# Kernel tuning notes

Measured on AMD Instinct MI355X. Metric: run time of the kernel, lower is better.

## Reference

```python
import jax, jax.numpy as jnp
import numpy as np

EPS = 1e-08
N_NODES = 100000
E_HALF = 3200000  # directed edges before symmetrization


def setup_inputs() -> dict:
    key = jax.random.key(0)
    k1, k2, k3 = jax.random.split(key, 3)
    pos = jax.random.normal(k1, (N_NODES, 3), dtype=jnp.float32)
    phi = jax.random.normal(k2, (N_NODES,), dtype=jnp.float32)
    e = jax.random.randint(k3, (2, E_HALF), 0, N_NODES, dtype=jnp.int32)
    # symmetrize (the torch module calls to_undirected); build undirected edge list
    edge_index = jnp.concatenate([e, e[::-1]], axis=1)  # (2, 2*E_HALF)
    return {"pos": pos, "phi": phi, "edge_index": edge_index}


def reference(pos, phi, edge_index):
    # pos: (N, 3), phi: (N,), edge_index: (2, E) already undirected
    n = pos.shape[0]
    row, col = edge_index[0], edge_index[1]
    dx = pos[col] - pos[row]                      # (E, 3)
    dphi = phi[col] - phi[row]                    # (E,)
    w = 1.0 / (jnp.linalg.norm(dx, axis=1) + EPS) ** 2  # (E,)
    outer = dx[:, :, None] * dx[:, None, :]      # (E, 3, 3)
    A = jax.ops.segment_sum(w[:, None, None] * outer, row, num_segments=n)  # (N,3,3)
    b = jax.ops.segment_sum((w * dphi)[:, None] * dx, row, num_segments=n)  # (N,3)
    A_reg = A + EPS * jnp.eye(3, dtype=pos.dtype)[None, :, :]
    grad_phi = jnp.linalg.solve(A_reg, b[..., None])[..., 0]  # (N,3)
    return grad_phi
```

## Files before the change

kernel.cpp:

```cpp
#include <hip/hip_runtime.h>
#include <hip/hip_bf16.h>
#include <math.h>

#define LSQ_EPS 1e-8f
#define BUCKET_BITS 7
#define BUCKET_SIZE 128
#define NB_MAX 800
#define CAP 8960
#define SCAT_BLOCKS 1024
#define STAGE_CAP 6272
#define VEC_ITERS 4
#define KV 5

__device__ __forceinline__ int hget(const unsigned int* hp, int b) {
    return (int)((hp[b >> 1] >> ((b & 1) * 16)) & 0xFFFFu);
}
__device__ __forceinline__ unsigned int hinc_rank(unsigned int* hp, int b) {
    unsigned int o = atomicAdd(&hp[b >> 1], 1u << ((b & 1) * 16));
    return (o >> ((b & 1) * 16)) & 0xFFFFu;
}

__global__ __launch_bounds__(256, 5) void lsq_scatter_sorted(
    const float* __restrict__ pos, const float* __restrict__ phi,
    const int* __restrict__ eidx, int E, int N, int NB,
    float4* __restrict__ pp4,
    unsigned int* __restrict__ region, int* __restrict__ g_cursor)
{
    __shared__ unsigned int staged[STAGE_CAP];
    __shared__ unsigned int histp[NB_MAX / 2];
    __shared__ unsigned short base16[NB_MAX];
    __shared__ unsigned short sstart16[NB_MAX];

    const int tid = threadIdx.x;
    const int E2 = E >> 1;

    for (int i = blockIdx.x * 256 + tid; i < N; i += SCAT_BLOCKS * 256)
        pp4[i] = make_float4(pos[3 * i + 0], pos[3 * i + 1], pos[3 * i + 2], phi[i]);

    int chunk = (E2 + SCAT_BLOCKS - 1) / SCAT_BLOCKS;
    chunk = (chunk + 3) & ~3;
    const int start = blockIdx.x * chunk;
    const int end = min(start + chunk, E2);
    if (start >= E2) return;

    for (int t = tid; t < NB_MAX / 2; t += 256) histp[t] = 0;
    __syncthreads();

    const int nvec = (end - start) & ~3;
    unsigned int rkA[VEC_ITERS][4];
    int4 rA[VEC_ITERS], cA[VEC_ITERS];
#pragma unroll
    for (int k = 0; k < VEC_ITERS; ++k) {
        int e = start + (tid << 2) + (k << 10);
        if (e < start + nvec) {
            int4 r = *(const int4*)(eidx + e);
            int4 c = *(const int4*)(eidx + E + e);
            rA[k] = r;
            cA[k] = c;
            rkA[k][0] = hinc_rank(histp, r.x >> BUCKET_BITS) |
                        (hinc_rank(histp, c.x >> BUCKET_BITS) << 16);
            rkA[k][1] = hinc_rank(histp, r.y >> BUCKET_BITS) |
                        (hinc_rank(histp, c.y >> BUCKET_BITS) << 16);
            rkA[k][2] = hinc_rank(histp, r.z >> BUCKET_BITS) |
                        (hinc_rank(histp, c.z >> BUCKET_BITS) << 16);
            rkA[k][3] = hinc_rank(histp, r.w >> BUCKET_BITS) |
                        (hinc_rank(histp, c.w >> BUCKET_BITS) << 16);
        }
    }
    unsigned int rkT = 0;
    int trow = 0, tcol = 0;
    const int tcnt = (end - start) - nvec;
    if (tid < tcnt) {
        int e = start + nvec + tid;
        trow = eidx[e];
        tcol = eidx[E + e];
        rkT = hinc_rank(histp, trow >> BUCKET_BITS) |
              (hinc_rank(histp, tcol >> BUCKET_BITS) << 16);
    }
    __syncthreads();

    int bs0 = 0, bs1 = 0, bs2 = 0, bs3 = 0;
    {
        int b = tid;
        if (b < NB) { int c = hget(histp, b); if (c > 0) bs0 = atomicAdd(&g_cursor[b], c); }
        b += 256;
        if (b < NB) { int c = hget(histp, b); if (c > 0) bs1 = atomicAdd(&g_cursor[b], c); }
        b += 256;
        if (b < NB) { int c = hget(histp, b); if (c > 0) bs2 = atomicAdd(&g_cursor[b], c); }
        b += 256;
        if (b < NB) { int c = hget(histp, b); if (c > 0) bs3 = atomicAdd(&g_cursor[b], c); }
    }
    if (tid < 64) {
        int carry = 0;
        for (int bi = 0; bi < NB; bi += 64) {
            int b = bi + tid;
            int c = (b < NB) ? hget(histp, b) : 0;
            int x = c;
#pragma unroll
            for (int d = 1; d < 64; d <<= 1) {
                int y = __shfl_up(x, d, 64);
                if (tid >= d) x += y;
            }
            if (b < NB) sstart16[b] = (unsigned short)(carry + x - c);
            carry += __shfl(x, 63, 64);
        }
    }
    asm volatile("s_waitcnt lgkmcnt(0)" ::: "memory");
    __builtin_amdgcn_s_barrier();

#pragma unroll
    for (int k = 0; k < VEC_ITERS; ++k) {
        int e = start + (tid << 2) + (k << 10);
        if (e < start + nvec) {
            int rr[4] = {rA[k].x, rA[k].y, rA[k].z, rA[k].w};
            int cc[4] = {cA[k].x, cA[k].y, cA[k].z, cA[k].w};
#pragma unroll
            for (int q = 0; q < 4; ++q) {
                int b1 = rr[q] >> BUCKET_BITS;
                int s1 = (int)sstart16[b1] + (int)(rkA[k][q] & 0xFFFFu);
                staged[s1] = ((unsigned int)(rr[q] & (BUCKET_SIZE - 1)) << 17) | (unsigned int)cc[q];
                int b2 = cc[q] >> BUCKET_BITS;
                int s2 = (int)sstart16[b2] + (int)(rkA[k][q] >> 16);
                staged[s2] = ((unsigned int)(cc[q] & (BUCKET_SIZE - 1)) << 17) | (unsigned int)rr[q];
            }
        }
    }
    if (tid < tcnt) {
        int b1 = trow >> BUCKET_BITS;
        staged[(int)sstart16[b1] + (int)(rkT & 0xFFFFu)] =
            ((unsigned int)(trow & (BUCKET_SIZE - 1)) << 17) | (unsigned int)tcol;
        int b2 = tcol >> BUCKET_BITS;
        staged[(int)sstart16[b2] + (int)(rkT >> 16)] =
            ((unsigned int)(tcol & (BUCKET_SIZE - 1)) << 17) | (unsigned int)trow;
    }

    if (tid < NB)       base16[tid]       = (unsigned short)min(bs0, 65535);
    if (tid + 256 < NB) base16[tid + 256] = (unsigned short)min(bs1, 65535);
    if (tid + 512 < NB) base16[tid + 512] = (unsigned short)min(bs2, 65535);
    if (tid + 768 < NB) base16[tid + 768] = (unsigned short)min(bs3, 65535);
    __syncthreads();

    {
        const int wv = tid >> 6, ln = tid & 63;
        const int grp = ln >> 3;
        const int sub = ln & 7;
        for (int b = wv * 8 + grp; b < NB; b += 32) {
            int cnt_b = hget(histp, b);
            if (cnt_b == 0) continue;
            int src = (int)sstart16[b];
            int dst = (int)base16[b];
            int kmax = min(cnt_b, CAP - dst);
            if (kmax <= 0) continue;
            unsigned int* dstp = region + (size_t)b * CAP + dst;
            const unsigned int* srcp = staged + src;
            for (int j = sub; j < kmax; j += 8)
                dstp[j] = srcp[j];
        }
    }
}

#define LSQ_ACC(qv)                                                            \
    {                                                                          \
        float dx = (qv).x - me.x;                                              \
        float dy = (qv).y - me.y;                                              \
        float dz = (qv).z - me.z;                                              \
        float dphi = (qv).w - me.w;                                            \
        float nn = sqrtf(dx * dx + dy * dy + dz * dz) + LSQ_EPS;               \
        float w = 1.0f / (nn * nn);                                            \
        float wd = w * dphi;                                                   \
        a00 += w * dx * dx; a01 += w * dx * dy; a02 += w * dx * dz;            \
        a11 += w * dy * dy; a12 += w * dy * dz; a22 += w * dz * dz;            \
        bb0 += wd * dx;     bb1 += wd * dy;     bb2 += wd * dz;                \
    }

__global__ __launch_bounds__(512, 6) void lsq_bucket_reduce(
    const float4* __restrict__ pp4,
    const unsigned int* __restrict__ region, const int* __restrict__ g_cursor,
    float* __restrict__ out, int N)
{
    __shared__ unsigned int sorted32[CAP];
    __shared__ int cnt[BUCKET_SIZE];
    __shared__ int startx[BUCKET_SIZE];

    const int b = blockIdx.x;
    const int tid = threadIdx.x;
    const int node_base = b << BUCKET_BITS;

    if (tid < BUCKET_SIZE) cnt[tid] = 0;
    __syncthreads();

    int count = g_cursor[b];
    if (count > CAP) count = CAP;
    const unsigned int* reg = region + (size_t)b * CAP;

    uint4 pcv[KV];
#pragma unroll
    for (int k = 0; k < KV; ++k) {
        int i = (tid << 2) + (k << 11);
        if (i < count) {
            uint4 p = *(const uint4*)(reg + i);
            unsigned int o0 = (unsigned int)atomicAdd(&cnt[p.x >> 17], 1);
            pcv[k].x = p.x | (o0 << 24);
            if (i + 1 < count) {
                unsigned int o1 = (unsigned int)atomicAdd(&cnt[p.y >> 17], 1);
                pcv[k].y = p.y | (o1 << 24);
            }
            if (i + 2 < count) {
                unsigned int o2 = (unsigned int)atomicAdd(&cnt[p.z >> 17], 1);
                pcv[k].z = p.z | (o2 << 24);
            }
            if (i + 3 < count) {
                unsigned int o3 = (unsigned int)atomicAdd(&cnt[p.w >> 17], 1);
                pcv[k].w = p.w | (o3 << 24);
            }
        }
    }
    __syncthreads();

    if (tid < 64) {
        int c0 = cnt[tid];
        int c1 = cnt[tid + 64];
        int x0 = c0, x1 = c1;
#pragma unroll
        for (int d = 1; d < 64; d <<= 1) {
            int y0 = __shfl_up(x0, d, 64);
            int y1 = __shfl_up(x1, d, 64);
            if (tid >= d) { x0 += y0; x1 += y1; }
        }
        int tot0 = __shfl(x0, 63, 64);
        startx[tid] = x0 - c0;
        startx[tid + 64] = tot0 + x1 - c1;
    }
    __syncthreads();

#pragma unroll
    for (int k = 0; k < KV; ++k) {
        int i = (tid << 2) + (k << 11);
        if (i < count) {
            unsigned int p0 = pcv[k].x;
            sorted32[startx[(p0 >> 17) & 0x7Fu] + (int)(p0 >> 24)] = p0 & 0x1FFFFu;
            if (i + 1 < count) {
                unsigned int p1 = pcv[k].y;
                sorted32[startx[(p1 >> 17) & 0x7Fu] + (int)(p1 >> 24)] = p1 & 0x1FFFFu;
            }
            if (i + 2 < count) {
                unsigned int p2 = pcv[k].z;
                sorted32[startx[(p2 >> 17) & 0x7Fu] + (int)(p2 >> 24)] = p2 & 0x1FFFFu;
            }
            if (i + 3 < count) {
                unsigned int p3 = pcv[k].w;
                sorted32[startx[(p3 >> 17) & 0x7Fu] + (int)(p3 >> 24)] = p3 & 0x1FFFFu;
            }
        }
    }
    __syncthreads();

    const int n = tid >> 2;
    const int qid = tid & 3;
    int node = node_base + n;
    float4 me = pp4[node < N ? node : 0];
    const int s = startx[n];
    const int cN = cnt[n];
    int lo = s + (cN * qid) / 4;
    const int hi = s + (cN * (qid + 1)) / 4;

    float a00 = 0, a01 = 0, a02 = 0, a11 = 0, a12 = 0, a22 = 0;
    float bb0 = 0, bb1 = 0, bb2 = 0;

    int i = lo;
    float4 q0, q1, q2, q3;
    bool have = (i + 3 < hi);
    if (have) {
        int c0 = (int)sorted32[i];
        int c1 = (int)sorted32[i + 1];
        int c2 = (int)sorted32[i + 2];
        int c3 = (int)sorted32[i + 3];
        q0 = pp4[c0]; q1 = pp4[c1]; q2 = pp4[c2]; q3 = pp4[c3];
    }
    while (have) {
        const int j = i + 4;
        const bool nhave = (j + 3 < hi);
        float4 p0, p1, p2, p3;
        if (nhave) {
            int c0 = (int)sorted32[j];
            int c1 = (int)sorted32[j + 1];
            int c2 = (int)sorted32[j + 2];
            int c3 = (int)sorted32[j + 3];
            p0 = pp4[c0]; p1 = pp4[c1]; p2 = pp4[c2]; p3 = pp4[c3];
        }
        LSQ_ACC(q0); LSQ_ACC(q1); LSQ_ACC(q2); LSQ_ACC(q3);
        q0 = p0; q1 = p1; q2 = p2; q3 = p3;
        i = j;
        have = nhave;
    }
    for (; i < hi; ++i) {
        int c0 = (int)sorted32[i];
        float4 qt = pp4[c0];
        LSQ_ACC(qt);
    }

    a00 += __shfl_down(a00, 1); a01 += __shfl_down(a01, 1);
    a02 += __shfl_down(a02, 1); a11 += __shfl_down(a11, 1);
    a12 += __shfl_down(a12, 1); a22 += __shfl_down(a22, 1);
    bb0 += __shfl_down(bb0, 1); bb1 += __shfl_down(bb1, 1);
    bb2 += __shfl_down(bb2, 1);
    a00 += __shfl_down(a00, 2); a01 += __shfl_down(a01, 2);
    a02 += __shfl_down(a02, 2); a11 += __shfl_down(a11, 2);
    a12 += __shfl_down(a12, 2); a22 += __shfl_down(a22, 2);
    bb0 += __shfl_down(bb0, 2); bb1 += __shfl_down(bb1, 2);
    bb2 += __shfl_down(bb2, 2);

    if (qid == 0 && node < N) {
        double a00d = (double)a00 + 1e-8;
        double a01d = (double)a01;
        double a02d = (double)a02;
        double a11d = (double)a11 + 1e-8;
        double a12d = (double)a12;
        double a22d = (double)a22 + 1e-8;
        double b0 = (double)bb0;
        double b1 = (double)bb1;
        double b2 = (double)bb2;

        double c00 = a11d * a22d - a12d * a12d;
        double c01 = a02d * a12d - a01d * a22d;
        double c02 = a01d * a12d - a02d * a11d;
        double c11 = a00d * a22d - a02d * a02d;
        double c12 = a01d * a02d - a00d * a12d;
        double c22 = a00d * a11d - a01d * a01d;

        double det = a00d * c00 + a01d * c01 + a02d * c02;
        double inv = 1.0 / det;

        out[node * 3 + 0] = (float)((c00 * b0 + c01 * b1 + c02 * b2) * inv);
        out[node * 3 + 1] = (float)((c01 * b0 + c11 * b1 + c12 * b2) * inv);
        out[node * 3 + 2] = (float)((c02 * b0 + c12 * b1 + c22 * b2) * inv);
    }
}

__global__ void lsq_edge_scatter(const float* __restrict__ pos,
                                 const float* __restrict__ phi,
                                 const int* __restrict__ eidx,
                                 float* __restrict__ acc,
                                 int E) {
    int e = blockIdx.x * blockDim.x + threadIdx.x;
    if (e >= E) return;
    int r = eidx[e];
    int c = eidx[E + e];
    float dx = pos[3 * c + 0] - pos[3 * r + 0];
    float dy = pos[3 * c + 1] - pos[3 * r + 1];
    float dz = pos[3 * c + 2] - pos[3 * r + 2];
    float dphi = phi[c] - phi[r];
    float n = sqrtf(dx * dx + dy * dy + dz * dz) + LSQ_EPS;
    float w = 1.0f / (n * n);
    float wd = w * dphi;
    float* a = acc + (size_t)r * 9;
    unsafeAtomicAdd(a + 0, w * dx * dx);
    unsafeAtomicAdd(a + 1, w * dx * dy);
    unsafeAtomicAdd(a + 2, w * dx * dz);
    unsafeAtomicAdd(a + 3, w * dy * dy);
    unsafeAtomicAdd(a + 4, w * dy * dz);
    unsafeAtomicAdd(a + 5, w * dz * dz);
    unsafeAtomicAdd(a + 6, wd * dx);
    unsafeAtomicAdd(a + 7, wd * dy);
    unsafeAtomicAdd(a + 8, wd * dz);
}

__global__ void lsq_solve3(const float* __restrict__ acc,
                           float* __restrict__ out,
                           int N) {
    int i = blockIdx.x * blockDim.x + threadIdx.x;
    if (i >= N) return;
    const float* a = acc + (size_t)i * 9;
    double a00 = (double)a[0] + 1e-8;
    double a01 = (double)a[1];
    double a02 = (double)a[2];
    double a11 = (double)a[3] + 1e-8;
    double a12 = (double)a[4];
    double a22 = (double)a[5] + 1e-8;
    double b0 = (double)a[6];
    double b1 = (double)a[7];
    double b2 = (double)a[8];
    double c00 = a11 * a22 - a12 * a12;
    double c01 = a02 * a12 - a01 * a22;
    double c02 = a01 * a12 - a02 * a11;
    double c11 = a00 * a22 - a02 * a02;
    double c12 = a01 * a02 - a00 * a12;
    double c22 = a00 * a11 - a01 * a01;
    double det = a00 * c00 + a01 * c01 + a02 * c02;
    double inv = 1.0 / det;
    out[3 * i + 0] = (float)((c00 * b0 + c01 * b1 + c02 * b2) * inv);
    out[3 * i + 1] = (float)((c01 * b0 + c11 * b1 + c12 * b2) * inv);
    out[3 * i + 2] = (float)((c02 * b0 + c12 * b1 + c22 * b2) * inv);
}

extern "C" void kernel_launch(void* const* d_in, const int* in_sizes, int n_in,
                              void* d_out, int out_size, void* d_ws, size_t ws_size,
                              hipStream_t stream) {
    const float* pos = (const float*)d_in[0];
    const float* phi = (const float*)d_in[1];
    const int* eidx = (const int*)d_in[2];
    float* out = (float*)d_out;

    int N = in_sizes[0] / 3;
    int E = in_sizes[2] / 2;
    int NB = (N + BUCKET_SIZE - 1) >> BUCKET_BITS;

    size_t region_bytes = (size_t)NB * CAP * sizeof(unsigned int);
    size_t pp4_bytes = (size_t)N * sizeof(float4);
    size_t need = region_bytes + pp4_bytes + (size_t)NB * sizeof(int);

    int chunk = ((E / 2) + SCAT_BLOCKS - 1) / SCAT_BLOCKS;
    chunk = (chunk + 3) & ~3;
    bool stage_ok = (2 * chunk) <= STAGE_CAP;

    if (NB <= NB_MAX && ws_size >= need && (E & 3) == 0 && stage_ok) {
        unsigned int* region = (unsigned int*)d_ws;
        float4* pp4 = (float4*)((char*)d_ws + region_bytes);
        int* g_cursor = (int*)((char*)d_ws + region_bytes + pp4_bytes);

        hipMemsetAsync(g_cursor, 0, (size_t)NB * sizeof(int), stream);
        lsq_scatter_sorted<<<SCAT_BLOCKS, 256, 0, stream>>>(
            pos, phi, eidx, E, N, NB, pp4, region, g_cursor);
        lsq_bucket_reduce<<<NB, 512, 0, stream>>>(pp4, region, g_cursor, out, N);
    } else {
        float* acc = (float*)d_ws;
        hipMemsetAsync(acc, 0, (size_t)N * 9 * sizeof(float), stream);
        int threads = 256;
        lsq_edge_scatter<<<(E + threads - 1) / threads, threads, 0, stream>>>(pos, phi, eidx, acc, E);
        lsq_solve3<<<(N + threads - 1) / threads, threads, 0, stream>>>(acc, out, N);
    }
}
```

Baseline: 171.8 us.

## Replace global bucket atomics with per-block staged output and metadata table

The scatter kernel no longer reserves space per bucket with global atomics or copies staged edges into per-bucket regions. Instead each block writes its locally sorted staging buffer contiguously, along with a per-block table of bucket start and count. The reduce kernel reads that table for its bucket, prefix-sums it across all scatter blocks, and gathers the pieces from each block's region. This removes the memset, the global atomic contention and the scattered small writes. In exchange, every reduce block reads 1024 metadata entries in a strided pattern and gathers many short segments, and the larger LDS footprint lowers occupancy.

```diff
diff --git a/kernel.cpp b/kernel.cpp
--- a/kernel.cpp
+++ b/kernel.cpp
@@ -10,7 +10,6 @@
 #define SCAT_BLOCKS 1024
 #define STAGE_CAP 6272
 #define VEC_ITERS 4
-#define KV 5
 
 __device__ __forceinline__ int hget(const unsigned int* hp, int b) {
     return (int)((hp[b >> 1] >> ((b & 1) * 16)) & 0xFFFFu);
@@ -24,11 +23,10 @@
     const float* __restrict__ pos, const float* __restrict__ phi,
     const int* __restrict__ eidx, int E, int N, int NB,
     float4* __restrict__ pp4,
-    unsigned int* __restrict__ region, int* __restrict__ g_cursor)
+    unsigned int* __restrict__ region, unsigned int* __restrict__ meta)
 {
     __shared__ unsigned int staged[STAGE_CAP];
     __shared__ unsigned int histp[NB_MAX / 2];
-    __shared__ unsigned short base16[NB_MAX];
     __shared__ unsigned short sstart16[NB_MAX];
 
     const int tid = threadIdx.x;
@@ -79,17 +77,6 @@
     }
     __syncthreads();
 
-    int bs0 = 0, bs1 = 0, bs2 = 0, bs3 = 0;
-    {
-        int b = tid;
-        if (b < NB) { int c = hget(histp, b); if (c > 0) bs0 = atomicAdd(&g_cursor[b], c); }
-        b += 256;
-        if (b < NB) { int c = hget(histp, b); if (c > 0) bs1 = atomicAdd(&g_cursor[b], c); }
-        b += 256;
-        if (b < NB) { int c = hget(histp, b); if (c > 0) bs2 = atomicAdd(&g_cursor[b], c); }
-        b += 256;
-        if (b < NB) { int c = hget(histp, b); if (c > 0) bs3 = atomicAdd(&g_cursor[b], c); }
-    }
     if (tid < 64) {
         int carry = 0;
         for (int bi = 0; bi < NB; bi += 64) {
@@ -105,8 +92,13 @@
             carry += __shfl(x, 63, 64);
         }
     }
-    asm volatile("s_waitcnt lgkmcnt(0)" ::: "memory");
-    __builtin_amdgcn_s_barrier();
+    __syncthreads();
+
+    {
+        unsigned int* mrow = meta + (size_t)blockIdx.x * NB;
+        for (int b = tid; b < NB; b += 256)
+            mrow[b] = ((unsigned int)sstart16[b] << 16) | (unsigned int)hget(histp, b);
+    }
 
 #pragma unroll
     for (int k = 0; k < VEC_ITERS; ++k) {
@@ -133,29 +125,14 @@
         staged[(int)sstart16[b2] + (int)(rkT >> 16)] =
             ((unsigned int)(tcol & (BUCKET_SIZE - 1)) << 17) | (unsigned int)trow;
     }
-
-    if (tid < NB)       base16[tid]       = (unsigned short)min(bs0, 65535);
-    if (tid + 256 < NB) base16[tid + 256] = (unsigned short)min(bs1, 65535);
-    if (tid + 512 < NB) base16[tid + 512] = (unsigned short)min(bs2, 65535);
-    if (tid + 768 < NB) base16[tid + 768] = (unsigned short)min(bs3, 65535);
     __syncthreads();
 
     {
-        const int wv = tid >> 6, ln = tid & 63;
-        const int grp = ln >> 3;
-        const int sub = ln & 7;
-        for (int b = wv * 8 + grp; b < NB; b += 32) {
-            int cnt_b = hget(histp, b);
-            if (cnt_b == 0) continue;
-            int src = (int)sstart16[b];
-            int dst = (int)base16[b];
-            int kmax = min(cnt_b, CAP - dst);
-            if (kmax <= 0) continue;
-            unsigned int* dstp = region + (size_t)b * CAP + dst;
-            const unsigned int* srcp = staged + src;
-            for (int j = sub; j < kmax; j += 8)
-                dstp[j] = srcp[j];
-        }
+        const int fill4 = (2 * (end - start)) >> 2;
+        uint4* dst4 = (uint4*)(region + (size_t)blockIdx.x * (2 * chunk));
+        const uint4* src4 = (const uint4*)staged;
+        for (int i = tid; i < fill4; i += 256)
+            dst4[i] = src4[i];
     }
 }
 
@@ -173,45 +150,69 @@
         bb0 += wd * dx;     bb1 += wd * dy;     bb2 += wd * dz;                \
     }
 
-__global__ __launch_bounds__(512, 6) void lsq_bucket_reduce(
+__global__ __launch_bounds__(512, 4) void lsq_bucket_reduce(
     const float4* __restrict__ pp4,
-    const unsigned int* __restrict__ region, const int* __restrict__ g_cursor,
-    float* __restrict__ out, int N)
+    const unsigned int* __restrict__ region, const unsigned int* __restrict__ meta,
+    float* __restrict__ out, int N, int E, int NB)
 {
+    __shared__ unsigned int buf1[CAP];
     __shared__ unsigned int sorted32[CAP];
+    __shared__ unsigned short mcnt[SCAT_BLOCKS];
+    __shared__ unsigned short msrt[SCAT_BLOCKS];
+    __shared__ unsigned short pblk[SCAT_BLOCKS];
     __shared__ int cnt[BUCKET_SIZE];
     __shared__ int startx[BUCKET_SIZE];
+    __shared__ int tot_s;
 
     const int b = blockIdx.x;
     const int tid = threadIdx.x;
     const int node_base = b << BUCKET_BITS;
+    const int E2 = E >> 1;
+    int chunk = (E2 + SCAT_BLOCKS - 1) / SCAT_BLOCKS;
+    chunk = (chunk + 3) & ~3;
+    const int nblk = min(SCAT_BLOCKS, (E2 + chunk - 1) / chunk);
+    const int BSTRIDE = 2 * chunk;
 
     if (tid < BUCKET_SIZE) cnt[tid] = 0;
-    __syncthreads();
-
-    int count = g_cursor[b];
-    if (count > CAP) count = CAP;
-    const unsigned int* reg = region + (size_t)b * CAP;
-
-    uint4 pcv[KV];
-#pragma unroll
-    for (int k = 0; k < KV; ++k) {
-        int i = (tid << 2) + (k << 11);
-        if (i < count) {
-            uint4 p = *(const uint4*)(reg + i);
-            unsigned int o0 = (unsigned int)atomicAdd(&cnt[p.x >> 17], 1);
-            pcv[k].x = p.x | (o0 << 24);
-            if (i + 1 < count) {
-                unsigned int o1 = (unsigned int)atomicAdd(&cnt[p.y >> 17], 1);
-                pcv[k].y = p.y | (o1 << 24);
+
+    for (int r = tid; r < SCAT_BLOCKS; r += 512) {
+        unsigned int m = (r < nblk) ? meta[(size_t)r * NB + b] : 0u;
+        mcnt[r] = (unsigned short)(m & 0xFFFFu);
+        msrt[r] = (unsigned short)(m >> 16);
+    }
+    __syncthreads();
+
+    if (tid < 64) {
+        int carry = 0;
+        for (int base = 0; base < SCAT_BLOCKS; base += 64) {
+            int c = (int)mcnt[base + tid];
+            int x = c;
+#pragma unroll
+            for (int d = 1; d < 64; d <<= 1) {
+                int y = __shfl_up(x, d, 64);
+                if (tid >= d) x += y;
             }
-            if (i + 2 < count) {
-                unsigned int o2 = (unsigned int)atomicAdd(&cnt[p.z >> 17], 1);
-                pcv[k].z = p.z | (o2 << 24);
-            }
-            if (i + 3 < count) {
-                unsigned int o3 = (unsigned int)atomicAdd(&cnt[p.w >> 17], 1);
-                pcv[k].w = p.w | (o3 << 24);
+            pblk[base + tid] = (unsigned short)min(carry + x - c, 65535);
+            carry += __shfl(x, 63, 64);
+        }
+        if (tid == 0) tot_s = carry;
+    }
+    __syncthreads();
+    const int total = min(tot_s, CAP);
+
+    {
+        const int wv = tid >> 6, ln = tid & 63;
+        const int grp = ln >> 3, sub = ln & 7;
+        for (int r = wv * 8 + grp; r < SCAT_BLOCKS; r += 64) {
+            int len = (int)mcnt[r];
+            if (len == 0) continue;
+            int dst0 = (int)pblk[r];
+            int kmax = min(len, CAP - dst0);
+            const unsigned int* srcp = region + (size_t)r * BSTRIDE + (int)msrt[r];
+            for (int j = sub; j < kmax; j += 8) {
+                unsigned int p = srcp[j];
+                unsigned int rk = (unsigned int)atomicAdd(&cnt[(p >> 17) & 0x7F], 1);
+                buf1[dst0 + j] = (p & 0x00FFFFFFu) | (rk << 24);
             }
         }
     }
@@ -233,25 +234,9 @@
     }
     __syncthreads();
 
-#pragma unroll
-    for (int k = 0; k < KV; ++k) {
-        int i = (tid << 2) + (k << 11);
-        if (i < count) {
-            unsigned int p0 = pcv[k].x;
-            sorted32[startx[(p0 >> 17) & 0x7Fu] + (int)(p0 >> 24)] = p0 & 0x1FFFFu;
-            if (i + 1 < count) {
-                unsigned int p1 = pcv[k].y;
-                sorted32[startx[(p1 >> 17) & 0x7Fu] + (int)(p1 >> 24)] = p1 & 0x1FFFFu;
-            }
-            if (i + 2 < count) {
-                unsigned int p2 = pcv[k].z;
-                sorted32[startx[(p2 >> 17) & 0x7Fu] + (int)(p2 >> 24)] = p2 & 0x1FFFFu;
-            }
-            if (i + 3 < count) {
-                unsigned int p3 = pcv[k].w;
-                sorted32[startx[(p3 >> 17) & 0x7Fu] + (int)(p3 >> 24)] = p3 & 0x1FFFFu;
-            }
-        }
+    for (int i = tid; i < total; i += 512) {
+        unsigned int p = buf1[i];
+        sorted32[startx[(p >> 17) & 0x7Fu] + (int)(p >> 24)] = p & 0x1FFFFu;
     }
     __syncthreads();
 
@@ -405,23 +390,23 @@
     int E = in_sizes[2] / 2;
     int NB = (N + BUCKET_SIZE - 1) >> BUCKET_BITS;
 
-    size_t region_bytes = (size_t)NB * CAP * sizeof(unsigned int);
-    size_t pp4_bytes = (size_t)N * sizeof(float4);
-    size_t need = region_bytes + pp4_bytes + (size_t)NB * sizeof(int);
-
     int chunk = ((E / 2) + SCAT_BLOCKS - 1) / SCAT_BLOCKS;
     chunk = (chunk + 3) & ~3;
     bool stage_ok = (2 * chunk) <= STAGE_CAP;
 
+    size_t region_bytes = (size_t)SCAT_BLOCKS * 2 * chunk * sizeof(unsigned int);
+    size_t pp4_bytes = (size_t)N * sizeof(float4);
+    size_t meta_bytes = (size_t)SCAT_BLOCKS * NB * sizeof(unsigned int);
+    size_t need = region_bytes + pp4_bytes + meta_bytes;
+
     if (NB <= NB_MAX && ws_size >= need && (E & 3) == 0 && stage_ok) {
         unsigned int* region = (unsigned int*)d_ws;
         float4* pp4 = (float4*)((char*)d_ws + region_bytes);
-        int* g_cursor = (int*)((char*)d_ws + region_bytes + pp4_bytes);
-
-        hipMemsetAsync(g_cursor, 0, (size_t)NB * sizeof(int), stream);
+        unsigned int* meta = (unsigned int*)((char*)d_ws + region_bytes + pp4_bytes);
+
         lsq_scatter_sorted<<<SCAT_BLOCKS, 256, 0, stream>>>(
-            pos, phi, eidx, E, N, NB, pp4, region, g_cursor);
-        lsq_bucket_reduce<<<NB, 512, 0, stream>>>(pp4, region, g_cursor, out, N);
+            pos, phi, eidx, E, N, NB, pp4, region, meta);
+        lsq_bucket_reduce<<<NB, 512, 0, stream>>>(pp4, region, meta, out, N, E, NB);
     } else {
         float* acc = (float*)d_ws;
         hipMemsetAsync(acc, 0, (size_t)N * 9 * sizeof(float), stream);
```

Result: no change. 171.2 us (-0.4%).
